# Kernel optimization log

Hardware: AMD Instinct MI355X
Metric: run time of the kernel (lower is better)

The kernel has to match this reference:

```python
import jax, jax.numpy as jnp
import numpy as np

D_MODEL = 1024
D_INNER = 2048   # expand * d_model
D_STATE = 16
DT_RANK = 64     # ceil(d_model / 16)
D_CONV = 4
L = 2048
EPS = 1e-5


def setup_inputs() -> dict:
    key = jax.random.key(0)
    ks = jax.random.split(key, 8)
    sc = lambda k, shape: jax.random.normal(k, shape, jnp.float32) * 0.02
    A = jnp.tile(jnp.arange(1, D_STATE + 1, dtype=jnp.float32), (D_INNER, 1))
    return {
        "x": jax.random.normal(ks[0], (L, D_MODEL), jnp.float32),
        "W_in": sc(ks[1], (D_MODEL, 2 * D_INNER)),          # in_proj (no bias)
        "W_conv": sc(ks[2], (D_CONV, D_INNER)),             # depthwise conv kernel
        "b_conv": jnp.zeros((D_INNER,), jnp.float32),
        "W_x": sc(ks[3], (D_INNER, DT_RANK + 2 * D_STATE)), # x_proj (no bias)
        "W_dt": sc(ks[4], (DT_RANK, D_INNER)),
        "b_dt": jnp.zeros((D_INNER,), jnp.float32),
        "A_log": jnp.log(A),
        "D": jnp.ones((D_INNER,), jnp.float32),
        "W_out": sc(ks[5], (D_INNER, D_MODEL)),             # out_proj (no bias)
        "ln_scale": jnp.ones((D_MODEL,), jnp.float32),
        "ln_bias": jnp.zeros((D_MODEL,), jnp.float32),
        "drop_key": 0,  # unused: training=False -> DropPath is identity
    }


def reference(x, W_in, W_conv, b_conv, W_x, W_dt, b_dt, A_log, D, W_out,
              ln_scale, ln_bias, drop_key):
    l = x.shape[0]
    # LayerNorm (flax default: mean/var over features)
    mu = jnp.mean(x, axis=-1, keepdims=True)
    var = jnp.mean(jnp.square(x), axis=-1, keepdims=True) - jnp.square(mu)
    xn = (x - mu) * jax.lax.rsqrt(var + EPS) * ln_scale + ln_bias

    # MambaBlock
    xr = xn @ W_in                         # (l, 2*d_inner)
    u, res = xr[:, :D_INNER], xr[:, D_INNER:]

    # causal depthwise conv: pad left d_conv-1, take first l outputs
    up = jnp.pad(u, ((D_CONV - 1, 0), (0, 0)))
    uc = b_conv + sum(up[k:k + l] * W_conv[k] for k in range(D_CONV))
    u2 = jax.nn.silu(uc)                   # (l, d_inner)

    # SSM params (input-dependent)
    x_dbl = u2 @ W_x                       # (l, dt_rank + 2n)
    dt = x_dbl[:, :DT_RANK]
    B = x_dbl[:, DT_RANK:DT_RANK + D_STATE]
    C = x_dbl[:, DT_RANK + D_STATE:]
    delta = jax.nn.softplus(dt @ W_dt + b_dt)   # (l, d_inner)
    A = -jnp.exp(A_log)                         # (d_inner, n)

    dA = jnp.exp(jnp.einsum('ld,dn->ldn', delta, A))   # (l, d_inner, n)
    dBu = jnp.einsum('ld,ln->ldn', delta * u2, B)       # (l, d_inner, n)

    def step(h, inp):
        dA_t, dBu_t, C_t = inp
        h = dA_t * h + dBu_t               # (d_inner, n)
        return h, h @ C_t                  # y_t: (d_inner,)

    h0 = jnp.zeros((D_INNER, D_STATE), dtype=u2.dtype)
    _, ys = jax.lax.scan(step, h0, (dA, dBu, C))
    y = ys + u2 * D                        # (l, d_inner)

    y = y * jax.nn.silu(res)
    out = y @ W_out                        # (l, d_model)
    return out + x                         # residual (DropPath identity in eval)
```

## Files before the change

kernel.cpp:

```cpp
#include <hip/hip_runtime.h>
#include <math.h>

#define L_SEQ 2048
#define DM 1024
#define DI 2048
#define DS 16
#define DTR 64
#define EPS 1e-5f
#define NSEG 32
#define SEGLEN 64
#define NSTATE (DI * DS)

typedef float f32x4 __attribute__((ext_vector_type(4)));
typedef __bf16 bf16x8 __attribute__((ext_vector_type(8)));
typedef _Float16 h16x2 __attribute__((ext_vector_type(2)));

static __device__ __forceinline__ unsigned short f2bf(float f) {
  union { float f; unsigned u; } v; v.f = f;
  unsigned r = v.u + 0x7fffu + ((v.u >> 16) & 1u);
  return (unsigned short)(r >> 16);
}
static __device__ __forceinline__ float bf2f(unsigned short s) {
  union { unsigned u; float f; } v; v.u = ((unsigned)s) << 16;
  return v.f;
}

static __device__ __forceinline__ void gload16(const void* g, void* l) {
  __builtin_amdgcn_global_load_lds(
      (__attribute__((address_space(1))) void*)(unsigned long long)(g),
      (__attribute__((address_space(3))) void*)(unsigned)(unsigned long long)(l),
      16, 0, 0);
}

static __device__ __forceinline__ void trans_tile(
    const float* __restrict__ W, unsigned short* __restrict__ Wt,
    int K, int N, int n0, int k0)
{
  __shared__ unsigned short s[64][80];
  int tid = threadIdx.x;
  #pragma unroll
  for (int p = 0; p < 4; ++p) {
    int i = p * 16 + (tid >> 4);
    int j = (tid & 15) * 4;
    float4 w = *(const float4*)&W[(size_t)(k0 + i) * N + n0 + j];
    s[j + 0][i] = f2bf(w.x); s[j + 1][i] = f2bf(w.y);
    s[j + 2][i] = f2bf(w.z); s[j + 3][i] = f2bf(w.w);
  }
  __syncthreads();
  #pragma unroll
  for (int q = 0; q < 2; ++q) {
    int n = q * 32 + (tid >> 3);
    int i8 = (tid & 7) * 8;
    *(int4*)&Wt[(size_t)(n0 + n) * K + k0 + i8] = *(const int4*)&s[n][i8];
  }
}

__global__ __launch_bounds__(256) void prep_all(
    const float* __restrict__ x, const float* __restrict__ ln_s,
    const float* __restrict__ ln_b, unsigned short* __restrict__ xnb,
    const float* __restrict__ W_in, const float* __restrict__ W_out,
    const float* __restrict__ W_dt, const float* __restrict__ Wx,
    unsigned short* __restrict__ Wtin, unsigned short* __restrict__ Wtout,
    unsigned short* __restrict__ Wdt_t, unsigned short* __restrict__ Wxt)
{
  int b = blockIdx.x;
  int t = threadIdx.x;
  if (b < 2048) {
    __shared__ float red[8];
    int row = b;
    float4 xv = ((const float4*)(x + (size_t)row * DM))[t];
    float s  = xv.x + xv.y + xv.z + xv.w;
    float s2 = xv.x*xv.x + xv.y*xv.y + xv.z*xv.z + xv.w*xv.w;
    #pragma unroll
    for (int m = 32; m >= 1; m >>= 1) {
      s  += __shfl_xor(s, m);
      s2 += __shfl_xor(s2, m);
    }
    int wid = t >> 6, lane = t & 63;
    if (lane == 0) { red[wid] = s; red[4 + wid] = s2; }
    __syncthreads();
    s  = red[0] + red[1] + red[2] + red[3];
    s2 = red[4] + red[5] + red[6] + red[7];
    float mu = s * (1.f / DM);
    float var = s2 * (1.f / DM) - mu * mu;
    float rs = rsqrtf(var + EPS);
    float4 sc4 = ((const float4*)ln_s)[t];
    float4 bi4 = ((const float4*)ln_b)[t];
    ushort4 ob;
    ob.x = f2bf((xv.x - mu) * rs * sc4.x + bi4.x);
    ob.y = f2bf((xv.y - mu) * rs * sc4.y + bi4.y);
    ob.z = f2bf((xv.z - mu) * rs * sc4.z + bi4.z);
    ob.w = f2bf((xv.w - mu) * rs * sc4.w + bi4.w);
    *(ushort4*)&xnb[(size_t)row * DM + t * 4] = ob;
  } else if (b < 3072) {
    int r = b - 2048;
    trans_tile(W_in, Wtin, DM, 2 * DI, (r & 63) * 64, (r >> 6) * 64);
  } else if (b < 3584) {
    int r = b - 3072;
    trans_tile(W_out, Wtout, DI, DM, (r & 15) * 64, (r >> 4) * 64);
  } else if (b < 3616) {
    int r = b - 3584;
    trans_tile(W_dt, Wdt_t, DTR, DI, r * 64, 0);
  } else {
    int r = b - 3616;
    int i = r * 256 + t;
    #pragma unroll
    for (int p = 0; p < 64; ++p) {
      int ii = i + p * 4096;
      int n = ii >> 11, k = ii & 2047;
      Wxt[ii] = (n < 96) ? f2bf(Wx[(size_t)k * 96 + n]) : (unsigned short)0;
    }
  }
}

template<int BM, int BN, int EPI, int OUTB, int SPLITK, int PIPE>
__global__ __launch_bounds__(256) void gemm2(
    const unsigned short* __restrict__ A, int lda,
    const unsigned short* __restrict__ Bt, int ldb,
    void* __restrict__ Cv, int ldc,
    int M, int N, int K,
    const float* __restrict__ bias,
    const float* __restrict__ R, int ldr)
{
  constexpr int WM = BM / 2, WN = BN / 2;
  constexpr int FM = WM / 16, FN = WN / 16;
  constexpr int BUFE = (BM + BN) * 64;
  __shared__ __align__(16) unsigned short sm[BUFE * (PIPE ? 2 : 1)];

  int nwg = gridDim.x * gridDim.y;
  int bid = blockIdx.y * gridDim.x + blockIdx.x;
  if ((nwg & 7) == 0) {
    int cpx = nwg >> 3;
    bid = (bid & 7) * cpx + (bid >> 3);
  }
  int bx = bid % gridDim.x;
  int by = bid / gridDim.x;
  int m0 = by * BM, n0 = bx * BN;

  int tid = threadIdx.x;
  int lane = tid & 63, wid = tid >> 6;
  int wm = wid >> 1, wn = wid & 1;

  int kb = blockIdx.z * (K / SPLITK);
  int nt = (K / SPLITK) / 64;

  int rs = lane >> 3;
  int cs = (lane & 7) * 8;

  f32x4 acc[FM][FN];
  #pragma unroll
  for (int m = 0; m < FM; ++m)
    #pragma unroll
    for (int n = 0; n < FN; ++n) acc[m][n] = (f32x4){0.f, 0.f, 0.f, 0.f};

  auto STAGE = [&](int kt, int buf) {
    unsigned short* bA = sm + buf * BUFE;
    unsigned short* bB = bA + BM * 64;
    #pragma unroll
    for (int i = 0; i < BM / 32; ++i) {
      int chunk = wid * (BM / 32) + i;
      gload16(A + (size_t)(m0 + chunk * 8 + rs) * lda + kb + kt * 64 + cs,
              (char*)bA + chunk * 1024);
    }
    #pragma unroll
    for (int i = 0; i < BN / 32; ++i) {
      int chunk = wid * (BN / 32) + i;
      gload16(Bt + (size_t)(n0 + chunk * 8 + rs) * ldb + kb + kt * 64 + cs,
              (char*)bB + chunk * 1024);
    }
  };

  auto COMPUTE = [&](const unsigned short* bA, const unsigned short* bB) {
    #pragma unroll
    for (int kk = 0; kk < 2; ++kk) {
      bf16x8 aF[FM], bF[FN];
      #pragma unroll
      for (int m = 0; m < FM; ++m) {
        int r = wm * WM + m * 16 + (lane & 15);
        aF[m] = *(const bf16x8*)((const char*)bA + r * 128 + kk * 64 + (lane >> 4) * 16);
      }
      #pragma unroll
      for (int n = 0; n < FN; ++n) {
        int r = wn * WN + n * 16 + (lane & 15);
        bF[n] = *(const bf16x8*)((const char*)bB + r * 128 + kk * 64 + (lane >> 4) * 16);
      }
      #pragma unroll
      for (int m = 0; m < FM; ++m)
        #pragma unroll
        for (int n = 0; n < FN; ++n)
          acc[m][n] = __builtin_amdgcn_mfma_f32_16x16x32_bf16(
              aF[m], bF[n], acc[m][n], 0, 0, 0);
    }
  };

  if (PIPE) {
    STAGE(0, 0);
    __syncthreads();
    int cur = 0;
    for (int kt = 0; kt < nt; ++kt) {
      if (kt + 1 < nt) STAGE(kt + 1, cur ^ 1);
      COMPUTE(sm + cur * BUFE, sm + cur * BUFE + BM * 64);
      __syncthreads();
      cur ^= 1;
    }
  } else {
    for (int kt = 0; kt < nt; ++kt) {
      __syncthreads();
      STAGE(kt, 0);
      __syncthreads();
      COMPUTE(sm, sm + BM * 64);
    }
    __syncthreads();
  }

  int cm = (lane >> 4) * 4, cn = lane & 15;
  if (OUTB) {
    unsigned short* Cb = (unsigned short*)Cv;
    __syncthreads();
    #pragma unroll
    for (int m = 0; m < FM; ++m)
      #pragma unroll
      for (int n = 0; n < FN; ++n) {
        int col = wn * WN + n * 16 + cn;
        #pragma unroll
        for (int r = 0; r < 4; ++r) {
          int row = wm * WM + m * 16 + cm + r;
          float v = acc[m][n][r];
          if (EPI == 1) {
            float w = v + bias[m0 + row];
            v = (w > 20.f) ? w : log1pf(__expf(w));
          }
          sm[row * BN + col] = f2bf(v);
        }
      }
    __syncthreads();
    constexpr int NI4 = BM * BN / 8;
    for (int k = tid; k < NI4; k += 256) {
      int row = k / (BN / 8);
      int c8 = (k % (BN / 8)) * 8;
      *(int4*)&Cb[(size_t)(m0 + row) * ldc + n0 + c8] = *(const int4*)&sm[row * BN + c8];
    }
  } else {
    float* Cf = (float*)Cv + (size_t)blockIdx.z * M * ldc;
    #pragma unroll
    for (int m = 0; m < FM; ++m)
      #pragma unroll
      for (int n = 0; n < FN; ++n) {
        int col = n0 + wn * WN + n * 16 + cn;
        #pragma unroll
        for (int r = 0; r < 4; ++r) {
          int row = m0 + wm * WM + m * 16 + cm + r;
          float v = acc[m][n][r];
          if (EPI == 1) {
            float w = v + bias[row];
            v = (w > 20.f) ? w : log1pf(__expf(w));
          }
          if (EPI == 2) v += R[(size_t)row * ldr + col];
          Cf[(size_t)row * ldc + col] = v;
        }
      }
  }
}

__global__ __launch_bounds__(256) void xdbl_reduce(
    const float* __restrict__ part, unsigned short* __restrict__ xdbl)
{
  int i = (blockIdx.x * 256 + threadIdx.x) * 4;
  const int SL = 2048 * 128;
  float4 s = *(const float4*)&part[i];
  #pragma unroll
  for (int z = 1; z < 8; ++z) {
    float4 p = *(const float4*)&part[(size_t)z * SL + i];
    s.x += p.x; s.y += p.y; s.z += p.z; s.w += p.w;
  }
  ushort4 ob;
  ob.x = f2bf(s.x); ob.y = f2bf(s.y); ob.z = f2bf(s.z); ob.w = f2bf(s.w);
  *(ushort4*)&xdbl[i] = ob;
}

__global__ __launch_bounds__(256) void conv_silu_fused(
    const unsigned short* __restrict__ xrT,
    const float* __restrict__ Wc, const float* __restrict__ bc,
    unsigned short* __restrict__ u2T, unsigned short* __restrict__ u2b)
{
  __shared__ unsigned short st[128][68];
  int d0 = blockIdx.x * 64, l0 = blockIdx.y * 128;
  int tid = threadIdx.x;
  int dloc = tid & 63;
  int lp = (tid >> 6) * 32;
  int d = d0 + dloc;
  const unsigned short* ur = xrT + (size_t)d * L_SEQ + l0 + lp;
  float w0 = Wc[0 * DI + d], w1 = Wc[1 * DI + d];
  float w2 = Wc[2 * DI + d], w3 = Wc[3 * DI + d];
  float b = bc[d];

  ushort4 vin[8];
  #pragma unroll
  for (int j = 0; j < 8; ++j) vin[j] = *(const ushort4*)&ur[j * 4];
  ushort4 vh; vh.x = vh.y = vh.z = vh.w = 0;
  if (l0 + lp > 0) vh = *(const ushort4*)&ur[-4];
  float prev3 = bf2f(vh.y), prev2 = bf2f(vh.z), prev1 = bf2f(vh.w);

  #pragma unroll
  for (int j = 0; j < 8; ++j) {
    float xs[4] = {bf2f(vin[j].x), bf2f(vin[j].y), bf2f(vin[j].z), bf2f(vin[j].w)};
    ushort4 ob;
    unsigned short* o = (unsigned short*)&ob;
    #pragma unroll
    for (int i = 0; i < 4; ++i) {
      float y = b + w0 * prev3 + w1 * prev2 + w2 * prev1 + w3 * xs[i];
      prev3 = prev2; prev2 = prev1; prev1 = xs[i];
      float sig = 1.f / (1.f + __expf(-y));
      o[i] = f2bf(y * sig);
    }
    *(ushort4*)&u2T[(size_t)d * L_SEQ + l0 + lp + j * 4] = ob;
    st[lp + j * 4 + 0][dloc] = o[0];
    st[lp + j * 4 + 1][dloc] = o[1];
    st[lp + j * 4 + 2][dloc] = o[2];
    st[lp + j * 4 + 3][dloc] = o[3];
  }
  __syncthreads();
  int lr = tid >> 1, hf = (tid & 1) * 32;
  unsigned short* ob = &u2b[(size_t)(l0 + lr) * DI + d0 + hf];
  *(int4*)&ob[0]  = *(const int4*)&st[lr][hf + 0];
  *(int4*)&ob[8]  = *(const int4*)&st[lr][hf + 8];
  *(int4*)&ob[16] = *(const int4*)&st[lr][hf + 16];
  *(int4*)&ob[24] = *(const int4*)&st[lr][hf + 24];
}


__global__ __launch_bounds__(256) void scan_pass1(
    const unsigned short* __restrict__ deltaT, const unsigned short* __restrict__ u2T,
    const unsigned short* __restrict__ xdbl,
    const float* __restrict__ A_log,
    float* __restrict__ hend, float* __restrict__ aprod)
{
  int t = threadIdx.x;
  int ch = t >> 4, n = t & 15;
  int li = (t & 15) * 4;
  int d0 = blockIdx.x * 16, d = d0 + ch;
  int base = blockIdx.y * SEGLEN;

  __shared__ __align__(16) float sdT[16][68], suT[16][68], sBT[16][68];

  float An = -__expf(A_log[d * DS + n]);

  ushort4 rdu = *(const ushort4*)&deltaT[(size_t)d * L_SEQ + base + li];
  ushort4 ru  = *(const ushort4*)&u2T[(size_t)d * L_SEQ + base + li];
  int llb = t >> 2;
  int n4 = (t & 3) * 4;
  ushort4 rB = *(const ushort4*)&xdbl[(size_t)(base + llb) * 128 + 64 + n4];

  float d0v = bf2f(rdu.x), d1v = bf2f(rdu.y), d2v = bf2f(rdu.z), d3v = bf2f(rdu.w);
  sdT[ch][li + 0] = d0v; sdT[ch][li + 1] = d1v;
  sdT[ch][li + 2] = d2v; sdT[ch][li + 3] = d3v;
  suT[ch][li + 0] = d0v * bf2f(ru.x); suT[ch][li + 1] = d1v * bf2f(ru.y);
  suT[ch][li + 2] = d2v * bf2f(ru.z); suT[ch][li + 3] = d3v * bf2f(ru.w);
  sBT[n4 + 0][llb] = bf2f(rB.x); sBT[n4 + 1][llb] = bf2f(rB.y);
  sBT[n4 + 2][llb] = bf2f(rB.z); sBT[n4 + 3][llb] = bf2f(rB.w);
  __syncthreads();

  float h = 0.f, sdl = 0.f;
  #pragma unroll
  for (int g = 0; g < 64; g += 4) {
    float4 dl4 = *(const float4*)&sdT[ch][g];
    float4 du4 = *(const float4*)&suT[ch][g];
    float4 Bn4 = *(const float4*)&sBT[n][g];
    float dl[4] = {dl4.x, dl4.y, dl4.z, dl4.w};
    float du[4] = {du4.x, du4.y, du4.z, du4.w};
    float Bn[4] = {Bn4.x, Bn4.y, Bn4.z, Bn4.w};
    #pragma unroll
    for (int i = 0; i < 4; ++i) {
      float dA = __expf(dl[i] * An);
      sdl += dl[i];
      h = dA * h + du[i] * Bn[i];
    }
  }
  size_t idx = (size_t)blockIdx.y * NSTATE + d0 * DS + t;
  hend[idx]  = h;
  aprod[idx] = __expf(An * sdl);
}

__global__ __launch_bounds__(256) void scan_pass2(
    const float* __restrict__ hend, const float* __restrict__ aprod,
    float* __restrict__ h_in)
{
  int i = blockIdx.x * 256 + threadIdx.x;
  float h = 0.f;
  h_in[i] = 0.f;
  for (int s = 0; s < NSEG - 1; ++s) {
    h = aprod[(size_t)s * NSTATE + i] * h + hend[(size_t)s * NSTATE + i];
    h_in[(size_t)(s + 1) * NSTATE + i] = h;
  }
}

#define SVP 262
__global__ __launch_bounds__(256) void scan_pass3(
    const unsigned short* __restrict__ deltaT, const unsigned short* __restrict__ u2T,
    const unsigned short* __restrict__ resT,
    const unsigned short* __restrict__ xdbl,
    const float* __restrict__ A_log, const float* __restrict__ Dp,
    const float* __restrict__ h_in,
    unsigned short* __restrict__ yb)
{
  int t = threadIdx.x;
  int ch = t >> 4, n = t & 15;
  int li = (t & 15) * 4;
  int d0 = blockIdx.x * 16, d = d0 + ch;
  int s = blockIdx.y;
  int base = s * SEGLEN;

  __shared__ __align__(16) float sdT[16][68], suT[16][68];
  __shared__ __align__(16) float sBT[16][68], sCT[16][68];
  __shared__ __align__(4) _Float16 svh[32][SVP];
  __shared__ __align__(16) unsigned short syt[32][16];

  float An = -__expf(A_log[d * DS + n]);
  float h = h_in[(size_t)s * NSTATE + d0 * DS + t];

  ushort4 rdu = *(const ushort4*)&deltaT[(size_t)d * L_SEQ + base + li];
  ushort4 ru  = *(const ushort4*)&u2T[(size_t)d * L_SEQ + base + li];
  int llb = t >> 2;
  int n4 = (t & 3) * 4;
  ushort4 rB = *(const ushort4*)&xdbl[(size_t)(base + llb) * 128 + 64 + n4];
  ushort4 rC = *(const ushort4*)&xdbl[(size_t)(base + llb) * 128 + 80 + n4];

  float d0v = bf2f(rdu.x), d1v = bf2f(rdu.y), d2v = bf2f(rdu.z), d3v = bf2f(rdu.w);
  sdT[ch][li + 0] = d0v; sdT[ch][li + 1] = d1v;
  sdT[ch][li + 2] = d2v; sdT[ch][li + 3] = d3v;
  suT[ch][li + 0] = d0v * bf2f(ru.x); suT[ch][li + 1] = d1v * bf2f(ru.y);
  suT[ch][li + 2] = d2v * bf2f(ru.z); suT[ch][li + 3] = d3v * bf2f(ru.w);
  sBT[n4 + 0][llb] = bf2f(rB.x); sBT[n4 + 1][llb] = bf2f(rB.y);
  sBT[n4 + 2][llb] = bf2f(rB.z); sBT[n4 + 3][llb] = bf2f(rB.w);
  sCT[n4 + 0][llb] = bf2f(rC.x); sCT[n4 + 1][llb] = bf2f(rC.y);
  sCT[n4 + 2][llb] = bf2f(rC.z); sCT[n4 + 3][llb] = bf2f(rC.w);
  __syncthreads();

  #pragma unroll
  for (int half = 0; half < 2; ++half) {
    int g0 = half * 32;
    #pragma unroll
    for (int g = g0; g < g0 + 32; g += 4) {
      float4 dl4 = *(const float4*)&sdT[ch][g];
      float4 du4 = *(const float4*)&suT[ch][g];
      float4 Bn4 = *(const float4*)&sBT[n][g];
      float4 Cn4 = *(const float4*)&sCT[n][g];
      float dl[4] = {dl4.x, dl4.y, dl4.z, dl4.w};
      float du[4] = {du4.x, du4.y, du4.z, du4.w};
      float Bn[4] = {Bn4.x, Bn4.y, Bn4.z, Bn4.w};
      float Cn[4] = {Cn4.x, Cn4.y, Cn4.z, Cn4.w};
      #pragma unroll
      for (int i = 0; i < 4; ++i) {
        float dA = __expf(dl[i] * An);
        h = dA * h + du[i] * Bn[i];
        svh[g - g0 + i][t] = (_Float16)(h * Cn[i]);
      }
    }
    __syncthreads();

    #pragma unroll
    for (int r = 0; r < 2; ++r) {
      int idx = r * 256 + t;
      int ll = idx & 31, c2 = idx >> 5;
      const _Float16* row = &svh[ll][c2 * 16];
      float sum = 0.f;
      #pragma unroll
      for (int k = 0; k < 8; ++k) {
        h16x2 pv = *(const h16x2*)&row[k * 2];
        sum += (float)pv.x + (float)pv.y;
      }
      int dd = d0 + c2;
      int lg = base + g0 + ll;
      float uv = bf2f(u2T[(size_t)dd * L_SEQ + lg]);
      float rv = bf2f(resT[(size_t)dd * L_SEQ + lg]);
      float sig = 1.f / (1.f + __expf(-rv));
      syt[ll][c2] = f2bf((sum + uv * Dp[dd]) * rv * sig);
    }
    __syncthreads();
    if (t < 64) {
      int lr = t >> 1, hf = (t & 1) * 8;
      int lg = base + g0 + lr;
      *(int4*)&yb[(size_t)lg * DI + d0 + hf] = *(const int4*)&syt[lr][hf];
    }
    __syncthreads();
  }
}

extern "C" void kernel_launch(void* const* d_in, const int* in_sizes, int n_in,
                              void* d_out, int out_size, void* d_ws, size_t ws_size,
                              hipStream_t stream)
{
  const float* x      = (const float*)d_in[0];
  const float* W_in   = (const float*)d_in[1];
  const float* W_conv = (const float*)d_in[2];
  const float* b_conv = (const float*)d_in[3];
  const float* W_x    = (const float*)d_in[4];
  const float* W_dt   = (const float*)d_in[5];
  const float* b_dt   = (const float*)d_in[6];
  const float* A_log  = (const float*)d_in[7];
  const float* Dp     = (const float*)d_in[8];
  const float* W_out  = (const float*)d_in[9];
  const float* ln_s   = (const float*)d_in[10];
  const float* ln_b   = (const float*)d_in[11];

  char* ws = (char*)d_ws;
  const size_t MB = 1u << 20;
  unsigned short* xnb    = (unsigned short*)(ws);
  unsigned short* xrT    = (unsigned short*)(ws + 4 * MB);
  unsigned short* u2T    = (unsigned short*)(ws + 20 * MB);
  unsigned short* u2b    = (unsigned short*)(ws + 28 * MB);
  float*          hend   = (float*)(ws + 28 * MB);
  float*          aprod  = (float*)(ws + 32 * MB);
  unsigned short* xdbl   = (unsigned short*)(ws + 36 * MB);
  unsigned short* Wxt    = (unsigned short*)(ws + 36 * MB + 512 * 1024);
  unsigned short* Wdt_t  = (unsigned short*)(ws + 37 * MB);
  unsigned short* deltaTb= (unsigned short*)(ws + 38 * MB);
  unsigned short* Wtin   = (unsigned short*)(ws + 38 * MB);
  float*          part   = (float*)(ws + 46 * MB);
  float*          h_in   = (float*)(ws + 62 * MB);
  unsigned short* Wtout  = (unsigned short*)(ws + 66 * MB);
  unsigned short* yb     = (unsigned short*)(ws + 4 * MB);
  const unsigned short* resT = xrT + (size_t)DI * L_SEQ;

  prep_all<<<3632, 256, 0, stream>>>(x, ln_s, ln_b, xnb,
                                     W_in, W_out, W_dt, W_x,
                                     Wtin, Wtout, Wdt_t, Wxt);

  gemm2<128, 128, 0, 1, 1, 1><<<dim3(L_SEQ / 128, (2 * DI) / 128), 256, 0, stream>>>(
      Wtin, DM, xnb, DM, xrT, L_SEQ, 2 * DI, L_SEQ, DM, nullptr, nullptr, 0);

  conv_silu_fused<<<dim3(DI / 64, L_SEQ / 128), 256, 0, stream>>>(
      xrT, W_conv, b_conv, u2T, u2b);

  gemm2<64, 128, 0, 0, 8, 1><<<dim3(1, L_SEQ / 64, 8), 256, 0, stream>>>(
      u2b, DI, Wxt, DI, part, 128, L_SEQ, 128, DI, nullptr, nullptr, 0);

  xdbl_reduce<<<(L_SEQ * 128) / 1024, 256, 0, stream>>>(part, xdbl);

  gemm2<64, 128, 1, 1, 1, 0><<<dim3(L_SEQ / 128, DI / 64), 256, 0, stream>>>(
      Wdt_t, DTR, xdbl, 128, deltaTb, L_SEQ, DI, L_SEQ, DTR, b_dt, nullptr, 0);

  scan_pass1<<<dim3(DI / 16, NSEG - 1), 256, 0, stream>>>(
      deltaTb, u2T, xdbl, A_log, hend, aprod);

  scan_pass2<<<NSTATE / 256, 256, 0, stream>>>(hend, aprod, h_in);

  scan_pass3<<<dim3(DI / 16, NSEG), 256, 0, stream>>>(
      deltaTb, u2T, resT, xdbl, A_log, Dp, h_in, yb);

  gemm2<64, 64, 2, 0, 1, 1><<<dim3(DM / 64, L_SEQ / 64), 256, 0, stream>>>(
      yb, DI, Wtout, DI, (float*)d_out, DM, L_SEQ, DM, DI, nullptr, x, DM);
}
```

Baseline: 163.8 us.

## Fuse dt projection and softplus into scan passes, drop delta GEMM

Removes the separate GEMM that computed delta = softplus(dt @ W_dt + b_dt) into a global bf16 buffer. Scan_pass1 and scan_pass3 now each recompute their 16-channel by 64-step delta tile with MFMA bf16 instructions from xdbl and W_dt staged in shared memory, then apply softplus in place. This saves one kernel launch and the delta write/read round trip through global memory. In exchange the projection is computed twice, the scan kernels gain extra barriers and a one-wavefront MFMA phase, and pass3 reuses its svh shared buffer for staging. Delta is also now kept in fp32 instead of being rounded to bf16.

After: 185.4 us. 1.13x slower.

```diff
diff --git a/kernel.cpp b/kernel.cpp
--- a/kernel.cpp
+++ b/kernel.cpp
@@ -330,9 +330,10 @@
 
 
 __global__ __launch_bounds__(256) void scan_pass1(
-    const unsigned short* __restrict__ deltaT, const unsigned short* __restrict__ u2T,
+    const unsigned short* __restrict__ u2T,
     const unsigned short* __restrict__ xdbl,
     const float* __restrict__ A_log,
+    const unsigned short* __restrict__ Wdt_t, const float* __restrict__ b_dt,
     float* __restrict__ hend, float* __restrict__ aprod)
 {
   int t = threadIdx.x;
@@ -342,22 +343,60 @@
   int base = blockIdx.y * SEGLEN;
 
   __shared__ __align__(16) float sdT[16][68], suT[16][68], sBT[16][68];
+  __shared__ __align__(16) unsigned short sdt[64][72];
+  __shared__ __align__(16) unsigned short swd[16][72];
+  __shared__ float sbd[16];
 
   float An = -__expf(A_log[d * DS + n]);
 
-  ushort4 rdu = *(const ushort4*)&deltaT[(size_t)d * L_SEQ + base + li];
-  ushort4 ru  = *(const ushort4*)&u2T[(size_t)d * L_SEQ + base + li];
+  ushort4 ru = *(const ushort4*)&u2T[(size_t)d * L_SEQ + base + li];
   int llb = t >> 2;
   int n4 = (t & 3) * 4;
   ushort4 rB = *(const ushort4*)&xdbl[(size_t)(base + llb) * 128 + 64 + n4];
 
-  float d0v = bf2f(rdu.x), d1v = bf2f(rdu.y), d2v = bf2f(rdu.z), d3v = bf2f(rdu.w);
-  sdT[ch][li + 0] = d0v; sdT[ch][li + 1] = d1v;
-  sdT[ch][li + 2] = d2v; sdT[ch][li + 3] = d3v;
-  suT[ch][li + 0] = d0v * bf2f(ru.x); suT[ch][li + 1] = d1v * bf2f(ru.y);
-  suT[ch][li + 2] = d2v * bf2f(ru.z); suT[ch][li + 3] = d3v * bf2f(ru.w);
+  {
+    int kc = (t & 3) * 16;
+    *(int4*)&sdt[llb][kc]     = *(const int4*)&xdbl[(size_t)(base + llb) * 128 + kc];
+    *(int4*)&sdt[llb][kc + 8] = *(const int4*)&xdbl[(size_t)(base + llb) * 128 + kc + 8];
+    if (t < 64) {
+      *(int4*)&swd[t >> 2][kc]     = *(const int4*)&Wdt_t[(size_t)(d0 + (t >> 2)) * 64 + kc];
+      *(int4*)&swd[t >> 2][kc + 8] = *(const int4*)&Wdt_t[(size_t)(d0 + (t >> 2)) * 64 + kc + 8];
+    }
+    if (t < 16) sbd[t] = b_dt[d0 + t];
+  }
   sBT[n4 + 0][llb] = bf2f(rB.x); sBT[n4 + 1][llb] = bf2f(rB.y);
   sBT[n4 + 2][llb] = bf2f(rB.z); sBT[n4 + 3][llb] = bf2f(rB.w);
+  __syncthreads();
+
+  if (t < 64) {
+    int lane = t;
+    bf16x8 a0 = *(const bf16x8*)&swd[lane & 15][(lane >> 4) * 8];
+    bf16x8 a1 = *(const bf16x8*)&swd[lane & 15][32 + (lane >> 4) * 8];
+    #pragma unroll
+    for (int lt = 0; lt < 4; ++lt) {
+      bf16x8 b0 = *(const bf16x8*)&sdt[lt * 16 + (lane & 15)][(lane >> 4) * 8];
+      bf16x8 b1 = *(const bf16x8*)&sdt[lt * 16 + (lane & 15)][32 + (lane >> 4) * 8];
+      f32x4 dacc = (f32x4){0.f, 0.f, 0.f, 0.f};
+      dacc = __builtin_amdgcn_mfma_f32_16x16x32_bf16(a0, b0, dacc, 0, 0, 0);
+      dacc = __builtin_amdgcn_mfma_f32_16x16x32_bf16(a1, b1, dacc, 0, 0, 0);
+      int lcol = lt * 16 + (lane & 15);
+      #pragma unroll
+      for (int r = 0; r < 4; ++r) {
+        int drow = (lane >> 4) * 4 + r;
+        float w = dacc[r] + sbd[drow];
+        sdT[drow][lcol] = (w > 20.f) ? w : log1pf(__expf(w));
+      }
+    }
+  }
+  __syncthreads();
+
+  {
+    float4 dl4 = *(const float4*)&sdT[ch][li];
+    suT[ch][li + 0] = dl4.x * bf2f(ru.x);
+    suT[ch][li + 1] = dl4.y * bf2f(ru.y);
+    suT[ch][li + 2] = dl4.z * bf2f(ru.z);
+    suT[ch][li + 3] = dl4.w * bf2f(ru.w);
+  }
   __syncthreads();
 
   float h = 0.f, sdl = 0.f;
@@ -396,10 +435,11 @@
 
 #define SVP 262
 __global__ __launch_bounds__(256) void scan_pass3(
-    const unsigned short* __restrict__ deltaT, const unsigned short* __restrict__ u2T,
+    const unsigned short* __restrict__ u2T,
     const unsigned short* __restrict__ resT,
     const unsigned short* __restrict__ xdbl,
     const float* __restrict__ A_log, const float* __restrict__ Dp,
+    const unsigned short* __restrict__ Wdt_t, const float* __restrict__ b_dt,
     const float* __restrict__ h_in,
     unsigned short* __restrict__ yb)
 {
@@ -412,28 +452,67 @@
 
   __shared__ __align__(16) float sdT[16][68], suT[16][68];
   __shared__ __align__(16) float sBT[16][68], sCT[16][68];
-  __shared__ __align__(4) _Float16 svh[32][SVP];
+  __shared__ __align__(16) char ush[32 * SVP * 2];
   __shared__ __align__(16) unsigned short syt[32][16];
+  _Float16 (*svh)[SVP] = (_Float16(*)[SVP])ush;
+  unsigned short (*sdt)[72] = (unsigned short(*)[72])ush;
+  unsigned short (*swd)[72] = (unsigned short(*)[72])(ush + 64 * 72 * 2);
+  float* sbd = (float*)(ush + 64 * 72 * 2 + 16 * 72 * 2);
 
   float An = -__expf(A_log[d * DS + n]);
   float h = h_in[(size_t)s * NSTATE + d0 * DS + t];
 
-  ushort4 rdu = *(const ushort4*)&deltaT[(size_t)d * L_SEQ + base + li];
-  ushort4 ru  = *(const ushort4*)&u2T[(size_t)d * L_SEQ + base + li];
+  ushort4 ru = *(const ushort4*)&u2T[(size_t)d * L_SEQ + base + li];
   int llb = t >> 2;
   int n4 = (t & 3) * 4;
   ushort4 rB = *(const ushort4*)&xdbl[(size_t)(base + llb) * 128 + 64 + n4];
   ushort4 rC = *(const ushort4*)&xdbl[(size_t)(base + llb) * 128 + 80 + n4];
 
-  float d0v = bf2f(rdu.x), d1v = bf2f(rdu.y), d2v = bf2f(rdu.z), d3v = bf2f(rdu.w);
-  sdT[ch][li + 0] = d0v; sdT[ch][li + 1] = d1v;
-  sdT[ch][li + 2] = d2v; sdT[ch][li + 3] = d3v;
-  suT[ch][li + 0] = d0v * bf2f(ru.x); suT[ch][li + 1] = d1v * bf2f(ru.y);
-  suT[ch][li + 2] = d2v * bf2f(ru.z); suT[ch][li + 3] = d3v * bf2f(ru.w);
+  {
+    int kc = (t & 3) * 16;
+    *(int4*)&sdt[llb][kc]     = *(const int4*)&xdbl[(size_t)(base + llb) * 128 + kc];
+    *(int4*)&sdt[llb][kc + 8] = *(const int4*)&xdbl[(size_t)(base + llb) * 128 + kc + 8];
+    if (t < 64) {
+      *(int4*)&swd[t >> 2][kc]     = *(const int4*)&Wdt_t[(size_t)(d0 + (t >> 2)) * 64 + kc];
+      *(int4*)&swd[t >> 2][kc + 8] = *(const int4*)&Wdt_t[(size_t)(d0 + (t >> 2)) * 64 + kc + 8];
+    }
+    if (t < 16) sbd[t] = b_dt[d0 + t];
+  }
   sBT[n4 + 0][llb] = bf2f(rB.x); sBT[n4 + 1][llb] = bf2f(rB.y);
   sBT[n4 + 2][llb] = bf2f(rB.z); sBT[n4 + 3][llb] = bf2f(rB.w);
   sCT[n4 + 0][llb] = bf2f(rC.x); sCT[n4 + 1][llb] = bf2f(rC.y);
   sCT[n4 + 2][llb] = bf2f(rC.z); sCT[n4 + 3][llb] = bf2f(rC.w);
+  __syncthreads();
+
+  if (t < 64) {
+    int lane = t;
+    bf16x8 a0 = *(const bf16x8*)&swd[lane & 15][(lane >> 4) * 8];
+    bf16x8 a1 = *(const bf16x8*)&swd[lane & 15][32 + (lane >> 4) * 8];
+    #pragma unroll
+    for (int lt = 0; lt < 4; ++lt) {
+      bf16x8 b0 = *(const bf16x8*)&sdt[lt * 16 + (lane & 15)][(lane >> 4) * 8];
+      bf16x8 b1 = *(const bf16x8*)&sdt[lt * 16 + (lane & 15)][32 + (lane >> 4) * 8];
+      f32x4 dacc = (f32x4){0.f, 0.f, 0.f, 0.f};
+      dacc = __builtin_amdgcn_mfma_f32_16x16x32_bf16(a0, b0, dacc, 0, 0, 0);
+      dacc = __builtin_amdgcn_mfma_f32_16x16x32_bf16(a1, b1, dacc, 0, 0, 0);
+      int lcol = lt * 16 + (lane & 15);
+      #pragma unroll
+      for (int r = 0; r < 4; ++r) {
+        int drow = (lane >> 4) * 4 + r;
+        float w = dacc[r] + sbd[drow];
+        sdT[drow][lcol] = (w > 20.f) ? w : log1pf(__expf(w));
+      }
+    }
+  }
+  __syncthreads();
+
+  {
+    float4 dl4 = *(const float4*)&sdT[ch][li];
+    suT[ch][li + 0] = dl4.x * bf2f(ru.x);
+    suT[ch][li + 1] = dl4.y * bf2f(ru.y);
+    suT[ch][li + 2] = dl4.z * bf2f(ru.z);
+    suT[ch][li + 3] = dl4.w * bf2f(ru.w);
+  }
   __syncthreads();
 
   #pragma unroll
@@ -514,7 +593,6 @@
   unsigned short* xdbl   = (unsigned short*)(ws + 36 * MB);
   unsigned short* Wxt    = (unsigned short*)(ws + 36 * MB + 512 * 1024);
   unsigned short* Wdt_t  = (unsigned short*)(ws + 37 * MB);
-  unsigned short* deltaTb= (unsigned short*)(ws + 38 * MB);
   unsigned short* Wtin   = (unsigned short*)(ws + 38 * MB);
   float*          part   = (float*)(ws + 46 * MB);
   float*          h_in   = (float*)(ws + 62 * MB);
@@ -537,16 +615,13 @@
 
   xdbl_reduce<<<(L_SEQ * 128) / 1024, 256, 0, stream>>>(part, xdbl);
 
-  gemm2<64, 128, 1, 1, 1, 0><<<dim3(L_SEQ / 128, DI / 64), 256, 0, stream>>>(
-      Wdt_t, DTR, xdbl, 128, deltaTb, L_SEQ, DI, L_SEQ, DTR, b_dt, nullptr, 0);
-
   scan_pass1<<<dim3(DI / 16, NSEG - 1), 256, 0, stream>>>(
-      deltaTb, u2T, xdbl, A_log, hend, aprod);
+      u2T, xdbl, A_log, Wdt_t, b_dt, hend, aprod);
 
   scan_pass2<<<NSTATE / 256, 256, 0, stream>>>(hend, aprod, h_in);
 
   scan_pass3<<<dim3(DI / 16, NSEG), 256, 0, stream>>>(
-      deltaTb, u2T, resT, xdbl, A_log, Dp, h_in, yb);
+      u2T, resT, xdbl, A_log, Dp, Wdt_t, b_dt, h_in, yb);
 
   gemm2<64, 64, 2, 0, 1, 1><<<dim3(DM / 64, L_SEQ / 64), 256, 0, stream>>>(
       yb, DI, Wtout, DI, (float*)d_out, DM, L_SEQ, DM, DI, nullptr, x, DM);
```
